# Optimization experiments

Hardware: AMD Instinct MI355X
Metric: run time of the kernel (lower is better)

The kernel has to match this reference:

```python
import jax, jax.numpy as jnp
import numpy as np

N, T, H = 307, 256, 64
NH, DH = 4, 16  # transformer heads, head dim (64/4)


def _layernorm(x, g, b, eps=1e-5):
    mu = x.mean(-1, keepdims=True)
    var = ((x - mu) ** 2).mean(-1, keepdims=True)
    return (x - mu) / jnp.sqrt(var + eps) * g + b


def _run_cell(x, m, tf, tj, Anorm, W0, b0, W1, mixW, mixb, Wih, Whh, bih, bhh, outW, outb, jamW, jamb):
    # x,m,tf,tj: [N,T]. Per-timestep 4-path ChebConv(K=2) + softmax mixing + GRUCell.
    hidden = Whh.shape[1]

    def step(h, xs):
        x_t, m_t, tf_t, tj_t = xs  # each [N]
        msg_in = jnp.concatenate([h, m_t[:, None], tf_t[:, None], tj_t[:, None]], axis=-1)  # [N,H+3]
        am = Anorm @ msg_in  # [N,H+3]
        m_all = jnp.tanh(jnp.einsum('ni,poi->npo', msg_in, W0) + b0
                         + jnp.einsum('ni,poi->npo', am, W1))  # [N,4,H]
        mix = jax.nn.softmax(h @ mixW.T + mixb, axis=1)  # [N,4]
        msg = jnp.einsum('np,npo->no', mix, m_all)  # [N,H]
        inp = jnp.concatenate([msg, (x_t * m_t)[:, None], m_t[:, None]], axis=-1)  # [N,H+2]
        # PyTorch GRUCell (gate order r,z,n)
        gi = inp @ Wih.T + bih
        gh = h @ Whh.T + bhh
        i_r, i_z, i_n = jnp.split(gi, 3, axis=-1)
        h_r, h_z, h_n = jnp.split(gh, 3, axis=-1)
        r = jax.nn.sigmoid(i_r + h_r)
        z = jax.nn.sigmoid(i_z + h_z)
        n = jnp.tanh(i_n + r * h_n)
        h_new = (1.0 - z) * n + z * h
        h2 = h_new + 0.1 * h
        pred = (h2 @ outW.T + outb)[:, 0]
        jam = (h2 @ jamW.T + jamb)[:, 0]
        return h2, (pred, jam, h2)

    h0 = jnp.zeros((x.shape[0], hidden), x.dtype)
    _, (preds, jams, hs) = jax.lax.scan(step, h0, (x.T, m.T, tf.T, tj.T))
    return preds.T, jams.T, jnp.transpose(hs, (1, 0, 2))  # [N,T],[N,T],[N,T,H]


def _pos_enc(Tlen, hdim, dtype):
    pos = jnp.arange(Tlen, dtype=dtype)[:, None]
    div = 10000.0 ** (jnp.arange(0, hdim, 2, dtype=dtype) / hdim)
    pe = jnp.zeros((Tlen, hdim), dtype)
    pe = pe.at[:, 0::2].set(jnp.sin(pos / div))
    pe = pe.at[:, 1::2].set(jnp.cos(pos / div))
    return pe


def _enhancer(h, qkvW, qkvb, oW, ob, g1, be1, f1W, f1b, f2W, f2b, g2, be2, pW, pb):
    # h: [N,T,H]; post-norm TransformerEncoder (relu, no dropout at eval), then Linear(H,1)
    x = h + _pos_enc(h.shape[1], h.shape[2], h.dtype)[None]
    n_layers = qkvW.shape[0]
    for l in range(n_layers):
        qkv = x @ qkvW[l].T + qkvb[l]
        q, k, v = jnp.split(qkv, 3, axis=-1)
        sh = (x.shape[0], x.shape[1], NH, DH)
        q, k, v = q.reshape(sh), k.reshape(sh), v.reshape(sh)
        att = jax.nn.softmax(jnp.einsum('nqhd,nkhd->nhqk', q, k) / np.sqrt(DH).astype(np.float32), axis=-1)
        o = jnp.einsum('nhqk,nkhd->nqhd', att, v).reshape(x.shape)
        o = o @ oW[l].T + ob[l]
        x = _layernorm(x + o, g1[l], be1[l])
        f = jax.nn.relu(x @ f1W[l].T + f1b[l]) @ f2W[l].T + f2b[l]
        x = _layernorm(x + f, g2[l], be2[l])
    return (x @ pW.T + pb)[..., 0]  # [N,T]


def _forward(x_seq, m_seq, tod_free, tod_jam, Anorm,
             cell_chebW0, cell_chebb0, cell_chebW1, cell_mixW, cell_mixb,
             cell_Wih, cell_Whh, cell_bih, cell_bhh,
             cell_outW, cell_outb, cell_jamW, cell_jamb,
             fuse_W1, fuse_b1, fuse_W2, fuse_b2,
             tr_qkvW, tr_qkvb, tr_oW, tr_ob, tr_ln1g, tr_ln1b,
             tr_ff1W, tr_ff1b, tr_ff2W, tr_ff2b, tr_ln2g, tr_ln2b,
             tr_projW, tr_projb):
    def cell(i, x, m, tf, tj):
        return _run_cell(x, m, tf, tj, Anorm,
                         cell_chebW0[i], cell_chebb0[i], cell_chebW1[i],
                         cell_mixW[i], cell_mixb[i],
                         cell_Wih[i], cell_Whh[i], cell_bih[i], cell_bhh[i],
                         cell_outW[i], cell_outb[i], cell_jamW[i], cell_jamb[i])

    flip = lambda a: a[:, ::-1]
    pf, jf, h_fwd = cell(0, x_seq, m_seq, tod_free, tod_jam)
    pb_r, jb_r, h_bwd_r = cell(1, flip(x_seq), flip(m_seq), flip(tod_free), flip(tod_jam))
    pb, jb, h_bwd = flip(pb_r), flip(jb_r), h_bwd_r[:, ::-1]

    fuse_in = jnp.stack([pf, pb], axis=-1)  # [N,T,2]
    w = jax.nn.softmax(jax.nn.relu(fuse_in @ fuse_W1.T + fuse_b1) @ fuse_W2.T + fuse_b2, axis=-1)
    speed = w[..., 0] * pf + w[..., 1] * pb
    jam_logit = w[..., 0] * jf + w[..., 1] * jb

    h_fused = h_fwd * w[..., 0:1] + h_bwd * w[..., 1:2]  # [N,T,H]
    args = lambda i: (tr_qkvW[i], tr_qkvb[i], tr_oW[i], tr_ob[i], tr_ln1g[i], tr_ln1b[i],
                      tr_ff1W[i], tr_ff1b[i], tr_ff2W[i], tr_ff2b[i], tr_ln2g[i], tr_ln2b[i],
                      tr_projW[i], tr_projb[i])
    speed_refined = _enhancer(h_fused, *args(0))
    jam_refined = _enhancer(h_fused, *args(1))
    alpha = 0.3
    speed = (1.0 - alpha) * speed + alpha * speed_refined
    jam_logit = (1.0 - alpha) * jam_logit + alpha * jam_refined
    return speed, jam_logit


def setup_inputs() -> dict:
    key = jax.random.key(0)
    keys = list(jax.random.split(key, 40))
    kit = iter(keys)

    def rn(shape, s=0.05):
        return s * jax.random.normal(next(kit), shape, jnp.float32)

    # sparse gaussian-normalized adjacency -> row-normalized diffusion matrix
    rng = np.random.default_rng(0)
    d = rng.uniform(0.5, 3.0, (N, N)); d = (d + d.T) / 2
    keep = rng.uniform(size=(N, N)) < 0.05; keep = keep | keep.T
    d = np.where(keep, d, np.inf)
    sigma = d[d < np.inf].std() + 1e-8
    adj = np.where(d < np.inf, np.exp(-d ** 2 / sigma ** 2), 0.0)
    np.fill_diagonal(adj, 1.0)
    dinv = np.where(adj.sum(1) > 0, (adj.sum(1) + 1e-8) ** -0.5, 0.0)
    adj_sym = adj * dinv[:, None] * dinv[None, :]
    rowsum = adj_sym.sum(1)
    Anorm = (adj_sym * np.where(rowsum > 0, 1.0 / rowsum, 0.0)[:, None]).astype(np.float32)

    inp = {
        'x_seq': jax.random.normal(next(kit), (N, T), jnp.float32),
        'm_seq': (jax.random.uniform(next(kit), (N, T)) < 0.5).astype(jnp.float32),
        'tod_free': jax.random.uniform(next(kit), (N, T), jnp.float32),
        'tod_jam': jax.random.uniform(next(kit), (N, T), jnp.float32),
        'Anorm': jnp.asarray(Anorm),
        'cell_chebW0': rn((2, 4, H, H + 3)), 'cell_chebb0': jnp.zeros((2, 4, H), jnp.float32),
        'cell_chebW1': rn((2, 4, H, H + 3)),
        'cell_mixW': rn((2, 4, H)), 'cell_mixb': jnp.zeros((2, 4), jnp.float32),
        'cell_Wih': rn((2, 3 * H, H + 2)), 'cell_Whh': rn((2, 3 * H, H)),
        'cell_bih': jnp.zeros((2, 3 * H), jnp.float32), 'cell_bhh': jnp.zeros((2, 3 * H), jnp.float32),
        'cell_outW': rn((2, 1, H)), 'cell_outb': jnp.zeros((2, 1), jnp.float32),
        'cell_jamW': rn((2, 1, H)), 'cell_jamb': jnp.zeros((2, 1), jnp.float32),
        'fuse_W1': rn((H, 2)), 'fuse_b1': jnp.zeros((H,), jnp.float32),
        'fuse_W2': rn((2, H)), 'fuse_b2': jnp.zeros((2,), jnp.float32),
        'tr_qkvW': rn((2, 3, 3 * H, H)), 'tr_qkvb': jnp.zeros((2, 3, 3 * H), jnp.float32),
        'tr_oW': rn((2, 3, H, H)), 'tr_ob': jnp.zeros((2, 3, H), jnp.float32),
        'tr_ln1g': jnp.ones((2, 3, H), jnp.float32), 'tr_ln1b': jnp.zeros((2, 3, H), jnp.float32),
        'tr_ff1W': rn((2, 3, 256, H)), 'tr_ff1b': jnp.zeros((2, 3, 256), jnp.float32),
        'tr_ff2W': rn((2, 3, H, 256)), 'tr_ff2b': jnp.zeros((2, 3, H), jnp.float32),
        'tr_ln2g': jnp.ones((2, 3, H), jnp.float32), 'tr_ln2b': jnp.zeros((2, 3, H), jnp.float32),
        'tr_projW': rn((2, 1, H)), 'tr_projb': jnp.zeros((2, 1), jnp.float32),
    }
    return inp


def reference(x_seq, m_seq, tod_free, tod_jam, Anorm,
              cell_chebW0, cell_chebb0, cell_chebW1, cell_mixW, cell_mixb,
              cell_Wih, cell_Whh, cell_bih, cell_bhh,
              cell_outW, cell_outb, cell_jamW, cell_jamb,
              fuse_W1, fuse_b1, fuse_W2, fuse_b2,
              tr_qkvW, tr_qkvb, tr_oW, tr_ob, tr_ln1g, tr_ln1b,
              tr_ff1W, tr_ff1b, tr_ff2W, tr_ff2b, tr_ln2g, tr_ln2b,
              tr_projW, tr_projb):
    return _forward(x_seq, m_seq, tod_free, tod_jam, Anorm,
                    cell_chebW0, cell_chebb0, cell_chebW1, cell_mixW, cell_mixb,
                    cell_Wih, cell_Whh, cell_bih, cell_bhh,
                    cell_outW, cell_outb, cell_jamW, cell_jamb,
                    fuse_W1, fuse_b1, fuse_W2, fuse_b2,
                    tr_qkvW, tr_qkvb, tr_oW, tr_ob, tr_ln1g, tr_ln1b,
                    tr_ff1W, tr_ff1b, tr_ff2W, tr_ff2b, tr_ln2g, tr_ln2b,
                    tr_projW, tr_projb)
```

## Files before the change

### kernel.cpp

```cpp
#include <hip/hip_runtime.h>
#include <math.h>

#define NN   307
#define TT   256
#define HHH  64
#define NROW (NN*TT)
#define NBLK_D 77
#define SCANB  154

typedef unsigned short u16;
typedef __attribute__((ext_vector_type(8))) short short8;
typedef __attribute__((ext_vector_type(4))) float f4;

__device__ __forceinline__ float wsum(float v){
#pragma unroll
  for (int off = 32; off > 0; off >>= 1) v += __shfl_xor(v, off, 64);
  return v;
}
__device__ __forceinline__ float wsum16(float v){
#pragma unroll
  for (int off = 8; off > 0; off >>= 1) v += __shfl_xor(v, off, 64);
  return v;
}
__device__ __forceinline__ float ftanh(float x){
  x = fminf(20.f, fmaxf(-20.f, x));
  float e = __expf(2.f*x);
  return (e - 1.f)/(e + 1.f);
}
__device__ __forceinline__ float fsigm(float x){ return 1.f/(1.f + __expf(-x)); }

__device__ __forceinline__ u16 f2bf(float x){
  unsigned u = __float_as_uint(x);
  u += 0x7fffu + ((u >> 16) & 1u);
  return (u16)(u >> 16);
}
__device__ __forceinline__ void split8(const float* xv, short8& hi, short8& lo){
  union { short8 v; u16 u[8]; } H, L;
#pragma unroll
  for (int j = 0; j < 8; j++){
    const float x = xv[j];
    const u16 h = f2bf(x);
    H.u[j] = h;
    L.u[j] = f2bf(x - __uint_as_float((unsigned)h << 16));
  }
  hi = H.v; lo = L.v;
}

__global__ void k_sparse(const float* __restrict__ A, int* __restrict__ cnt,
                         int* __restrict__ idx, float* __restrict__ val){
  int n = blockIdx.x*64 + threadIdx.x;
  if (n >= NN) return;
  int c = 0;
  for (int m = 0; m < NN; m++){
    float a = A[n*NN + m];
    if (a != 0.f){ idx[n*NN + c] = m; val[n*NN + c] = a; c++; }
  }
  cnt[n] = c;
}

__global__ void k_tr_cheb(const float* __restrict__ W0, const float* __restrict__ W1,
                          float* __restrict__ W0T, float* __restrict__ W1T){
  int t = blockIdx.x*256 + threadIdx.x;
  if (t >= 2*67*256) return;
  int c = t & 255; int rest = t >> 8; int i = rest % 67; int d = rest / 67;
  int p = c >> 6, o = c & 63;
  int src = ((d*4 + p)*64 + o)*67 + i;
  W0T[t] = W0[src];
  W1T[t] = W1[src];
}

__global__ void k_tr_gru(const float* __restrict__ Wih, const float* __restrict__ Whh,
                         float* __restrict__ WihT, float* __restrict__ WhhT){
  int t = blockIdx.x*256 + threadIdx.x;
  if (t < 2*66*192){
    int j = t % 192; int rest = t / 192; int i = rest % 66; int d = rest / 66;
    WihT[t] = Wih[(d*192 + j)*66 + i];
  }
  if (t < 2*64*192){
    int j = t % 192; int rest = t / 192; int i = rest % 64; int d = rest / 64;
    WhhT[t] = Whh[(d*192 + j)*64 + i];
  }
}

__global__ void k_af(const float* __restrict__ mseq, const float* __restrict__ tfr,
                     const float* __restrict__ tjm, const int* __restrict__ cnt,
                     const int* __restrict__ idx, const float* __restrict__ val,
                     float* __restrict__ AF){
  int n = blockIdx.x, c = blockIdx.y, t = threadIdx.x;
  const float* feat = (c == 0) ? mseq : (c == 1) ? tfr : tjm;
  float acc = 0.f; int k = cnt[n];
  for (int s = 0; s < k; s++) acc += val[n*NN + s] * feat[idx[n*NN + s]*TT + t];
  AF[((size_t)c*NN + n)*TT + t] = acc;
}

__global__ void k_split(const float* __restrict__ src, u16* __restrict__ hi,
                        u16* __restrict__ lo, int n){
  int i = blockIdx.x*256 + threadIdx.x;
  if (i >= n) return;
  const float x = src[i];
  const u16 h = f2bf(x);
  hi[i] = h;
  lo[i] = f2bf(x - __uint_as_float((unsigned)h << 16));
}

__global__ __launch_bounds__(256, 1)
void k_scan(const float* __restrict__ xseq, const float* __restrict__ mseq,
            const float* __restrict__ tfr, const float* __restrict__ tjm,
            const float* __restrict__ W0T, const float* __restrict__ W1T,
            const float* __restrict__ b0g,
            const float* __restrict__ mixW, const float* __restrict__ mixb,
            const float* __restrict__ WihT, const float* __restrict__ WhhT,
            const float* __restrict__ bih, const float* __restrict__ bhh,
            const float* __restrict__ outW, const float* __restrict__ outb,
            const float* __restrict__ jamW, const float* __restrict__ jamb,
            const int* __restrict__ spcnt, const int* __restrict__ spidx,
            const float* __restrict__ spval, const float* __restrict__ AF,
            float* __restrict__ Hseq, float* __restrict__ PRED, float* __restrict__ JPRED,
            int* __restrict__ slots)
{
  const int tid = threadIdx.x;
  const int bid = blockIdx.x;
  const int d   = bid / NBLK_D;
  const int n0  = (bid % NBLK_D) * 4;
  const int lane = tid & 63;
  const int wid  = tid >> 6;

  __shared__ __align__(16) float hsT[64][4];
  __shared__ __align__(16) float amsT[68][4];
  __shared__ __align__(16) float msgsT[64][4];
  __shared__ float malls[256][5];
  __shared__ float gis[4][192];
  __shared__ float ghs[4][192];
  __shared__ float mixs[4][4];
  __shared__ float xss[4], mss[4], tfs[4], tjs[4];
  __shared__ int   s_idx[4][320];
  __shared__ float s_val[4][320];
  __shared__ int   s_cnt[4];

  float w0r[67], w1r[67];
#pragma unroll
  for (int i = 0; i < 67; i++){
    w0r[i] = W0T[(d*67 + i)*256 + tid];
    w1r[i] = W1T[(d*67 + i)*256 + tid];
  }
  const float b0r = b0g[d*256 + tid];
  float wih_r[64], whh_r[64];
  float wih64 = 0.f, wih65 = 0.f, bih_r = 0.f, bhh_r = 0.f;
  if (tid < 192){
#pragma unroll
    for (int i = 0; i < 64; i++){
      whh_r[i] = WhhT[(d*64 + i)*192 + tid];
      wih_r[i] = WihT[(d*66 + i)*192 + tid];
    }
    wih64 = WihT[(d*66 + 64)*192 + tid];
    wih65 = WihT[(d*66 + 65)*192 + tid];
    bih_r = bih[d*192 + tid];
    bhh_r = bhh[d*192 + tid];
  }
  float mixw_r[4];
#pragma unroll
  for (int p = 0; p < 4; p++) mixw_r[p] = mixW[(d*4 + p)*64 + lane];
  const float mixb0 = mixb[d*4+0], mixb1 = mixb[d*4+1], mixb2 = mixb[d*4+2], mixb3 = mixb[d*4+3];
  const float outw_r = outW[d*64 + lane], jamw_r = jamW[d*64 + lane];
  const float outb_r = outb[d], jamb_r = jamb[d];

  for (int r = 0; r < 4; r++){
    const int n = min(n0 + r, NN-1);
    const int cc = spcnt[n];
    const int ccp = (cc + 15) & ~15;
    if (tid == 0) s_cnt[r] = ccp;
    for (int s = tid; s < ccp; s += 256){
      s_idx[r][s] = (s < cc) ? spidx[n*NN + s] : 0;
      s_val[r][s] = (s < cc) ? spval[n*NN + s] : 0.f;
    }
  }
  hsT[lane][wid] = 0.f;
  __syncthreads();

#pragma unroll 1
  for (int k = 0; k < TT; k++){
    const int ts = (d == 0) ? k : (TT-1 - k);
    if (tid < 4){
      const int r = tid; const int n = min(n0 + r, NN-1);
      const float mv = mseq[n*TT + ts];
      mss[r] = mv; tfs[r] = tfr[n*TT + ts]; tjs[r] = tjm[n*TT + ts];
      xss[r] = xseq[n*TT + ts];
      amsT[64][r] = AF[(0*NN + n)*TT + ts];
      amsT[65][r] = AF[(1*NN + n)*TT + ts];
      amsT[66][r] = AF[(2*NN + n)*TT + ts];
    }
    {
      const int r = wid;
      const float hv = hsT[lane][r];
      float l0 = wsum(hv * mixw_r[0]) + mixb0;
      float l1 = wsum(hv * mixw_r[1]) + mixb1;
      float l2 = wsum(hv * mixw_r[2]) + mixb2;
      float l3 = wsum(hv * mixw_r[3]) + mixb3;
      const float mx = fmaxf(fmaxf(l0,l1), fmaxf(l2,l3));
      const float e0 = __expf(l0-mx), e1 = __expf(l1-mx), e2 = __expf(l2-mx), e3 = __expf(l3-mx);
      const float inv = 1.f/(e0+e1+e2+e3);
      if (lane == 0){
        mixs[0][r] = e0*inv; mixs[1][r] = e1*inv; mixs[2][r] = e2*inv; mixs[3][r] = e3*inv;
      }
    }
    __syncthreads();
    {
      float a0 = b0r, a1 = b0r, a2 = b0r, a3 = b0r;
#pragma unroll
      for (int i = 0; i < 64; i++){
        const float4 h4 = *(const float4*)&hsT[i][0];
        const float w = w0r[i];
        a0 += h4.x*w; a1 += h4.y*w; a2 += h4.z*w; a3 += h4.w*w;
      }
      a0 += mss[0]*w0r[64] + tfs[0]*w0r[65] + tjs[0]*w0r[66];
      a1 += mss[1]*w0r[64] + tfs[1]*w0r[65] + tjs[1]*w0r[66];
      a2 += mss[2]*w0r[64] + tfs[2]*w0r[65] + tjs[2]*w0r[66];
      a3 += mss[3]*w0r[64] + tfs[3]*w0r[65] + tjs[3]*w0r[66];
      malls[tid][0] = a0; malls[tid][1] = a1; malls[tid][2] = a2; malls[tid][3] = a3;
    }
    if (tid < 192){
      float g0 = bhh_r, g1 = bhh_r, g2 = bhh_r, g3 = bhh_r;
#pragma unroll
      for (int i = 0; i < 64; i++){
        const float4 h4 = *(const float4*)&hsT[i][0];
        const float w = whh_r[i];
        g0 += h4.x*w; g1 += h4.y*w; g2 += h4.z*w; g3 += h4.w*w;
      }
      ghs[0][tid] = g0; ghs[1][tid] = g1; ghs[2][tid] = g2; ghs[3][tid] = g3;
      gis[0][tid] = bih_r + (xss[0]*mss[0])*wih64 + mss[0]*wih65;
      gis[1][tid] = bih_r + (xss[1]*mss[1])*wih64 + mss[1]*wih65;
      gis[2][tid] = bih_r + (xss[2]*mss[2])*wih64 + mss[2]*wih65;
      gis[3][tid] = bih_r + (xss[3]*mss[3])*wih64 + mss[3]*wih65;
    }
    if (k > 0 && tid < 64){
      const int* sl = slots + (size_t)d*NBLK_D*16;
      const int i2 = lane + 64;
      for (;;){
        const int va = (lane < NBLK_D)
            ? __hip_atomic_load(&sl[lane*16], __ATOMIC_RELAXED, __HIP_MEMORY_SCOPE_AGENT)
            : 0x7fffffff;
        const int vb = (i2 < NBLK_D)
            ? __hip_atomic_load(&sl[i2*16], __ATOMIC_RELAXED, __HIP_MEMORY_SCOPE_AGENT)
            : 0x7fffffff;
        if (__all(min(va, vb) >= k)) break;
        __builtin_amdgcn_s_sleep(1);
      }
    }
    __syncthreads();
    {
      const float* Hprev = Hseq + (size_t)(d*257 + k)*NN*64;
      const int r = wid;
      const int ccp = s_cnt[r];
      float acc = 0.f;
      for (int s = 0; s < ccp; s += 16){
        float aV[16], hV[16];
#pragma unroll
        for (int u = 0; u < 16; u++){
          const int m = s_idx[r][s+u];
          aV[u] = s_val[r][s+u];
          hV[u] = __hip_atomic_load(&Hprev[(size_t)m*64 + lane],
                                    __ATOMIC_RELAXED, __HIP_MEMORY_SCOPE_AGENT);
        }
#pragma unroll
        for (int u = 0; u < 16; u++) acc += aV[u]*hV[u];
      }
      amsT[lane][r] = acc;
    }
    __syncthreads();
    {
      const int p = tid >> 6;
      float pa0 = malls[tid][0], pa1 = malls[tid][1], pa2 = malls[tid][2], pa3 = malls[tid][3];
#pragma unroll
      for (int i = 0; i < 67; i++){
        const float4 m4 = *(const float4*)&amsT[i][0];
        const float w = w1r[i];
        pa0 += m4.x*w; pa1 += m4.y*w; pa2 += m4.z*w; pa3 += m4.w*w;
      }
      malls[tid][0] = mixs[p][0]*ftanh(pa0);
      malls[tid][1] = mixs[p][1]*ftanh(pa1);
      malls[tid][2] = mixs[p][2]*ftanh(pa2);
      malls[tid][3] = mixs[p][3]*ftanh(pa3);
    }
    __syncthreads();
    msgsT[lane][wid] = malls[lane][wid] + malls[64+lane][wid] + malls[128+lane][wid] + malls[192+lane][wid];
    __syncthreads();
    if (tid < 192){
      float q0 = gis[0][tid], q1 = gis[1][tid], q2 = gis[2][tid], q3 = gis[3][tid];
#pragma unroll
      for (int i = 0; i < 64; i++){
        const float4 m4 = *(const float4*)&msgsT[i][0];
        const float w = wih_r[i];
        q0 += m4.x*w; q1 += m4.y*w; q2 += m4.z*w; q3 += m4.w*w;
      }
      gis[0][tid] = q0; gis[1][tid] = q1; gis[2][tid] = q2; gis[3][tid] = q3;
    }
    __syncthreads();
    {
      const int r = wid, o = lane;
      const float ir = gis[r][o], iz = gis[r][o+64], in_ = gis[r][o+128];
      const float hr = ghs[r][o], hz = ghs[r][o+64], hn = ghs[r][o+128];
      const float rr2 = fsigm(ir + hr);
      const float zz = fsigm(iz + hz);
      const float nnv = ftanh(in_ + rr2*hn);
      const float hold = hsT[o][r];
      const float h2 = (1.f - zz)*nnv + zz*hold + 0.1f*hold;
      hsT[o][r] = h2;
      const int n = n0 + r;
      if (n < NN)
        __hip_atomic_store(&Hseq[((size_t)(d*257 + k + 1)*NN + n)*64 + o], h2,
                           __ATOMIC_RELAXED, __HIP_MEMORY_SCOPE_AGENT);
    }
    __syncthreads();
    if (tid == 0)
      __hip_atomic_store(&slots[bid*16], k + 1, __ATOMIC_RELAXED, __HIP_MEMORY_SCOPE_AGENT);
    {
      const float h2 = hsT[lane][wid];
      const float pv = wsum(h2 * outw_r);
      const float jv = wsum(h2 * jamw_r);
      const int n = n0 + wid;
      if (lane == 0 && n < NN){
        PRED [(d*NN + n)*TT + ts] = pv + outb_r;
        JPRED[(d*NN + n)*TT + ts] = jv + jamb_r;
      }
    }
  }
}

__global__ __launch_bounds__(256)
void k_fusion(const float* __restrict__ PRED, const float* __restrict__ JPRED,
              const float* __restrict__ Hseq,
              const float* __restrict__ fw1, const float* __restrict__ fb1,
              const float* __restrict__ fw2, const float* __restrict__ fb2,
              float* __restrict__ x0, float* __restrict__ outp)
{
  const int tid = threadIdx.x;
  const int rr = tid >> 6, lane = tid & 63;
  const int idx = blockIdx.x*4 + rr;
  const int n = idx >> 8, t = idx & 255;
  const float pf = PRED[(0*NN + n)*TT + t], pb = PRED[(NN + n)*TT + t];
  const float jf = JPRED[(0*NN + n)*TT + t], jb = JPRED[(NN + n)*TT + t];
  const float hid = fmaxf(fw1[lane*2]*pf + fw1[lane*2+1]*pb + fb1[lane], 0.f);
  const float l0 = wsum(hid * fw2[lane]) + fb2[0];
  const float l1 = wsum(hid * fw2[64+lane]) + fb2[1];
  const float mx = fmaxf(l0,l1);
  const float e0 = __expf(l0-mx), e1 = __expf(l1-mx);
  const float inv = 1.f/(e0+e1);
  const float w0 = e0*inv, w1 = e1*inv;
  const float hf = Hseq[((size_t)(0*257 + t + 1)*NN + n)*64 + lane];
  const float hb = Hseq[((size_t)(257 + 256 - t)*NN + n)*64 + lane];
  const int i2 = lane & ~1;
  const float dv = powf(10000.f, (float)i2 * (1.f/64.f));
  const float arg = (float)t / dv;
  const float pe = (lane & 1) ? cosf(arg) : sinf(arg);
  x0[(size_t)idx*64 + lane] = hf*w0 + hb*w1 + pe;
  if (lane == 0){
    outp[idx]        = 0.7f*(w0*pf + w1*pb);
    outp[NROW + idx] = 0.7f*(w0*jf + w1*jb);
  }
}

__global__ __launch_bounds__(256)
void k_qkv(const float* __restrict__ X, const u16* __restrict__ Whi,
           const u16* __restrict__ Wlo, const float* __restrict__ bias,
           float* __restrict__ Y)
{
  const int tid = threadIdx.x;
  const int w = tid >> 6, l = tid & 63;
  const int m16 = l & 15, q = l >> 4;
  const int row = blockIdx.x*64 + w*16 + m16;
  short8 Ah[2], Al[2];
#pragma unroll
  for (int kh = 0; kh < 2; kh++){
    float xv[8];
    *(float4*)&xv[0] = *(const float4*)&X[(size_t)row*64 + kh*32 + q*8];
    *(float4*)&xv[4] = *(const float4*)&X[(size_t)row*64 + kh*32 + q*8 + 4];
    split8(xv, Ah[kh], Al[kh]);
  }
  const int rbase = blockIdx.x*64 + w*16 + q*4;
  for (int nt = 0; nt < 12; nt++){
    const int n = nt*16 + m16;
    f4 acc = {0.f, 0.f, 0.f, 0.f};
#pragma unroll
    for (int kh = 0; kh < 2; kh++){
      const short8 Bh = *(const short8*)&Whi[(size_t)n*64 + kh*32 + q*8];
      const short8 Bl = *(const short8*)&Wlo[(size_t)n*64 + kh*32 + q*8];
      acc = __builtin_amdgcn_mfma_f32_16x16x32_bf16(Ah[kh], Bh, acc, 0, 0, 0);
      acc = __builtin_amdgcn_mfma_f32_16x16x32_bf16(Ah[kh], Bl, acc, 0, 0, 0);
      acc = __builtin_amdgcn_mfma_f32_16x16x32_bf16(Al[kh], Bh, acc, 0, 0, 0);
    }
    const float bb = bias[n];
#pragma unroll
    for (int r = 0; r < 4; r++)
      Y[(size_t)(rbase + r)*192 + n] = acc[r] + bb;
  }
}

__global__ __launch_bounds__(256)
void k_oproj_ln(const float* __restrict__ X, const u16* __restrict__ Whi,
                const u16* __restrict__ Wlo, const float* __restrict__ bias,
                const float* __restrict__ Xres, const float* __restrict__ g,
                const float* __restrict__ b, float* __restrict__ Y)
{
  const int tid = threadIdx.x;
  const int w = tid >> 6, l = tid & 63;
  const int m16 = l & 15, q = l >> 4;
  const int row = blockIdx.x*64 + w*16 + m16;
  short8 Ah[2], Al[2];
#pragma unroll
  for (int kh = 0; kh < 2; kh++){
    float xv[8];
    *(float4*)&xv[0] = *(const float4*)&X[(size_t)row*64 + kh*32 + q*8];
    *(float4*)&xv[4] = *(const float4*)&X[(size_t)row*64 + kh*32 + q*8 + 4];
    split8(xv, Ah[kh], Al[kh]);
  }
  f4 acc[4];
#pragma unroll
  for (int nt = 0; nt < 4; nt++){
    acc[nt] = (f4){0.f, 0.f, 0.f, 0.f};
    const int n = nt*16 + m16;
#pragma unroll
    for (int kh = 0; kh < 2; kh++){
      const short8 Bh = *(const short8*)&Whi[(size_t)n*64 + kh*32 + q*8];
      const short8 Bl = *(const short8*)&Wlo[(size_t)n*64 + kh*32 + q*8];
      acc[nt] = __builtin_amdgcn_mfma_f32_16x16x32_bf16(Ah[kh], Bh, acc[nt], 0, 0, 0);
      acc[nt] = __builtin_amdgcn_mfma_f32_16x16x32_bf16(Ah[kh], Bl, acc[nt], 0, 0, 0);
      acc[nt] = __builtin_amdgcn_mfma_f32_16x16x32_bf16(Al[kh], Bh, acc[nt], 0, 0, 0);
    }
  }
  const int rbase = blockIdx.x*64 + w*16 + q*4;
#pragma unroll
  for (int r = 0; r < 4; r++){
    float v[4]; float s = 0.f;
#pragma unroll
    for (int nt = 0; nt < 4; nt++){
      const int col = nt*16 + m16;
      v[nt] = acc[nt][r] + bias[col] + Xres[(size_t)(rbase + r)*64 + col];
      s += v[nt];
    }
    const float mu = wsum16(s) * (1.f/64.f);
    float vs = 0.f;
#pragma unroll
    for (int nt = 0; nt < 4; nt++){ v[nt] -= mu; vs += v[nt]*v[nt]; }
    const float rstd = rsqrtf(wsum16(vs) * (1.f/64.f) + 1e-5f);
#pragma unroll
    for (int nt = 0; nt < 4; nt++){
      const int col = nt*16 + m16;
      Y[(size_t)(rbase + r)*64 + col] = v[nt] * rstd * g[col] + b[col];
    }
  }
}

__global__ __launch_bounds__(256)
void k_ffblock(const float* __restrict__ X,
               const u16* __restrict__ W1hi, const u16* __restrict__ W1lo,
               const float* __restrict__ b1,
               const u16* __restrict__ W2hi, const u16* __restrict__ W2lo,
               const float* __restrict__ b2,
               const float* __restrict__ g, const float* __restrict__ b,
               float* __restrict__ Y)
{
  __shared__ __align__(16) u16 Hs[64][280];
  const int tid = threadIdx.x;
  const int w = tid >> 6, l = tid & 63;
  const int m16 = l & 15, q = l >> 4;
  const int row = blockIdx.x*64 + w*16 + m16;
  short8 Ah[2], Al[2];
#pragma unroll
  for (int kh = 0; kh < 2; kh++){
    float xv[8];
    *(float4*)&xv[0] = *(const float4*)&X[(size_t)row*64 + kh*32 + q*8];
    *(float4*)&xv[4] = *(const float4*)&X[(size_t)row*64 + kh*32 + q*8 + 4];
    split8(xv, Ah[kh], Al[kh]);
  }
  for (int nt = 0; nt < 16; nt++){
    const int n = nt*16 + m16;
    f4 acc = {0.f, 0.f, 0.f, 0.f};
#pragma unroll
    for (int kh = 0; kh < 2; kh++){
      const short8 Bh = *(const short8*)&W1hi[(size_t)n*64 + kh*32 + q*8];
      const short8 Bl = *(const short8*)&W1lo[(size_t)n*64 + kh*32 + q*8];
      acc = __builtin_amdgcn_mfma_f32_16x16x32_bf16(Ah[kh], Bh, acc, 0, 0, 0);
      acc = __builtin_amdgcn_mfma_f32_16x16x32_bf16(Ah[kh], Bl, acc, 0, 0, 0);
      acc = __builtin_amdgcn_mfma_f32_16x16x32_bf16(Al[kh], Bh, acc, 0, 0, 0);
    }
    const float bb = b1[n];
#pragma unroll
    for (int r = 0; r < 4; r++){
      const float h = fmaxf(acc[r] + bb, 0.f);
      Hs[w*16 + q*4 + r][n] = f2bf(h);
    }
  }
  __syncthreads();
  f4 acc2[4];
#pragma unroll
  for (int nt = 0; nt < 4; nt++) acc2[nt] = (f4){0.f, 0.f, 0.f, 0.f};
#pragma unroll 1
  for (int kh = 0; kh < 8; kh++){
    const short8 Ahh = *(const short8*)&Hs[w*16 + m16][kh*32 + q*8];
#pragma unroll
    for (int nt = 0; nt < 4; nt++){
      const int n = nt*16 + m16;
      const short8 Bh = *(const short8*)&W2hi[(size_t)n*256 + kh*32 + q*8];
      const short8 Bl = *(const short8*)&W2lo[(size_t)n*256 + kh*32 + q*8];
      acc2[nt] = __builtin_amdgcn_mfma_f32_16x16x32_bf16(Ahh, Bh, acc2[nt], 0, 0, 0);
      acc2[nt] = __builtin_amdgcn_mfma_f32_16x16x32_bf16(Ahh, Bl, acc2[nt], 0, 0, 0);
    }
  }
  const int rbase = blockIdx.x*64 + w*16 + q*4;
#pragma unroll
  for (int r = 0; r < 4; r++){
    float v[4]; float s = 0.f;
#pragma unroll
    for (int nt = 0; nt < 4; nt++){
      const int col = nt*16 + m16;
      v[nt] = acc2[nt][r] + b2[col] + X[(size_t)(rbase + r)*64 + col];
      s += v[nt];
    }
    const float mu = wsum16(s) * (1.f/64.f);
    float vs = 0.f;
#pragma unroll
    for (int nt = 0; nt < 4; nt++){ v[nt] -= mu; vs += v[nt]*v[nt]; }
    const float rstd = rsqrtf(wsum16(vs) * (1.f/64.f) + 1e-5f);
#pragma unroll
    for (int nt = 0; nt < 4; nt++){
      const int col = nt*16 + m16;
      Y[(size_t)(rbase + r)*64 + col] = v[nt] * rstd * g[col] + b[col];
    }
  }
}

__global__ __launch_bounds__(256)
void k_attn(const float* __restrict__ QKV, float* __restrict__ O)
{
  const int n = blockIdx.x, h = blockIdx.y;
  const int tid = threadIdx.x;
  __shared__ __align__(16) float Ks[256][20];
  __shared__ __align__(16) float Vs[256][20];
  const float* nbase = QKV + (size_t)n*256*192;
  {
    const int part = tid & 7;
    const int kv = part >> 2;
    const int c4 = (part & 3) * 4;
#pragma unroll
    for (int p = 0; p < 8; p++){
      const int t = p*32 + (tid >> 3);
      const float4 v4 = *(const float4*)(nbase + (size_t)t*192 + 64 + kv*64 + h*16 + c4);
      if (kv == 0) *(float4*)&Ks[t][c4] = v4;
      else         *(float4*)&Vs[t][c4] = v4;
    }
  }
  float q[16];
  {
    const float4* qs = (const float4*)(nbase + (size_t)tid*192 + h*16);
#pragma unroll
    for (int c = 0; c < 4; c++){
      float4 t4 = qs[c];
      q[c*4+0]=t4.x*0.25f; q[c*4+1]=t4.y*0.25f; q[c*4+2]=t4.z*0.25f; q[c*4+3]=t4.w*0.25f;
    }
  }
  __syncthreads();
  float l = 0.f, acc[16] = {};
  for (int j = 0; j < 256; j++){
    float s = 0.f;
#pragma unroll
    for (int dd = 0; dd < 16; dd++) s += q[dd]*Ks[j][dd];
    const float p = __expf(s);
    l += p;
#pragma unroll
    for (int dd = 0; dd < 16; dd++) acc[dd] += p*Vs[j][dd];
  }
  const float inv = 1.f/l;
  float* orow = O + ((size_t)n*256 + tid)*64 + h*16;
#pragma unroll
  for (int dd = 0; dd < 16; dd++) orow[dd] = acc[dd]*inv;
}

__global__ __launch_bounds__(256)
void k_proj_add(const float* __restrict__ X, const float* __restrict__ pW,
                const float* __restrict__ pb, float* __restrict__ outp)
{
  const int tid = threadIdx.x;
  const int r = tid >> 6, lane = tid & 63;
  const size_t row = (size_t)blockIdx.x*4 + r;
  const float v = X[row*64 + lane] * pW[lane];
  const float s = wsum(v);
  if (lane == 0) outp[row] += 0.3f*(s + pb[0]);
}

extern "C" void kernel_launch(void* const* d_in, const int* in_sizes, int n_in,
                              void* d_out, int out_size, void* d_ws, size_t ws_size,
                              hipStream_t stream)
{
  const float* x_seq = (const float*)d_in[0];
  const float* m_seq = (const float*)d_in[1];
  const float* tod_f = (const float*)d_in[2];
  const float* tod_j = (const float*)d_in[3];
  const float* Anorm = (const float*)d_in[4];
  const float* chW0  = (const float*)d_in[5];
  const float* chb0  = (const float*)d_in[6];
  const float* chW1  = (const float*)d_in[7];
  const float* mixW  = (const float*)d_in[8];
  const float* mixb  = (const float*)d_in[9];
  const float* Wih   = (const float*)d_in[10];
  const float* Whh   = (const float*)d_in[11];
  const float* bih   = (const float*)d_in[12];
  const float* bhh   = (const float*)d_in[13];
  const float* outW  = (const float*)d_in[14];
  const float* outbp = (const float*)d_in[15];
  const float* jamW  = (const float*)d_in[16];
  const float* jambp = (const float*)d_in[17];
  const float* fW1   = (const float*)d_in[18];
  const float* fb1   = (const float*)d_in[19];
  const float* fW2   = (const float*)d_in[20];
  const float* fb2   = (const float*)d_in[21];
  const float* qkvW  = (const float*)d_in[22];
  const float* qkvb  = (const float*)d_in[23];
  const float* oW    = (const float*)d_in[24];
  const float* ob    = (const float*)d_in[25];
  const float* ln1g  = (const float*)d_in[26];
  const float* ln1b  = (const float*)d_in[27];
  const float* f1W   = (const float*)d_in[28];
  const float* f1b   = (const float*)d_in[29];
  const float* f2W   = (const float*)d_in[30];
  const float* f2b   = (const float*)d_in[31];
  const float* ln2g  = (const float*)d_in[32];
  const float* ln2b  = (const float*)d_in[33];
  const float* prW   = (const float*)d_in[34];
  const float* prb   = (const float*)d_in[35];
  float* out = (float*)d_out;

  float* ws = (float*)d_ws;
  size_t off = 0;
  auto take = [&](size_t n)->float*{ float* p = ws + off; off += (n + 63) & ~(size_t)63; return p; };
  int*   slots = (int*)take(4096);
  float* W0T  = take((size_t)2*67*256);
  float* W1T  = take((size_t)2*67*256);
  float* WihT = take((size_t)2*66*192);
  float* WhhT = take((size_t)2*64*192);
  int*   spcnt = (int*)take(320);
  int*   spidx = (int*)take((size_t)NN*NN);
  float* spval = take((size_t)NN*NN);
  float* AF    = take((size_t)3*NN*TT);
  float* PRED  = take((size_t)2*NN*TT);
  float* JPRED = take((size_t)2*NN*TT);
  float* HSEQ  = take((size_t)2*257*NN*64);
  float* X0    = take((size_t)NROW*64);
  float* XBUF  = take((size_t)NROW*64);
  float* OBUF  = take((size_t)NROW*64);
  float* FBUF  = take((size_t)NROW*256);
  const size_t NQKV = (size_t)6*192*64;
  const size_t NO   = (size_t)6*64*64;
  const size_t NF1  = (size_t)6*256*64;
  const size_t NF2  = (size_t)6*64*256;
  const size_t NWTOT = NQKV + NO + NF1 + NF2;
  u16* WHI = (u16*)take((NWTOT + 1)/2);
  u16* WLO = (u16*)take((NWTOT + 1)/2);
  (void)ws_size; (void)in_sizes; (void)n_in; (void)out_size;

  hipMemsetAsync(slots, 0, 4096*sizeof(int), stream);
  hipMemsetAsync(HSEQ, 0, (size_t)NN*64*sizeof(float), stream);
  hipMemsetAsync(HSEQ + (size_t)257*NN*64, 0, (size_t)NN*64*sizeof(float), stream);

  k_sparse<<<dim3((NN+63)/64), dim3(64), 0, stream>>>(Anorm, spcnt, spidx, spval);
  k_tr_cheb<<<dim3(134), dim3(256), 0, stream>>>(chW0, chW1, W0T, W1T);
  k_tr_gru<<<dim3(99), dim3(256), 0, stream>>>(Wih, Whh, WihT, WhhT);
  k_af<<<dim3(NN,3), dim3(256), 0, stream>>>(m_seq, tod_f, tod_j, spcnt, spidx, spval, AF);
  k_split<<<dim3((int)((NQKV+255)/256)), dim3(256), 0, stream>>>(qkvW, WHI, WLO, (int)NQKV);
  k_split<<<dim3((int)((NO+255)/256)), dim3(256), 0, stream>>>(oW, WHI+NQKV, WLO+NQKV, (int)NO);
  k_split<<<dim3((int)((NF1+255)/256)), dim3(256), 0, stream>>>(f1W, WHI+NQKV+NO, WLO+NQKV+NO, (int)NF1);
  k_split<<<dim3((int)((NF2+255)/256)), dim3(256), 0, stream>>>(f2W, WHI+NQKV+NO+NF1, WLO+NQKV+NO+NF1, (int)NF2);

  k_scan<<<dim3(SCANB), dim3(256), 0, stream>>>(x_seq, m_seq, tod_f, tod_j, W0T, W1T,
      chb0, mixW, mixb, WihT, WhhT, bih, bhh, outW, outbp, jamW, jambp,
      spcnt, spidx, spval, AF, HSEQ, PRED, JPRED, slots);

  k_fusion<<<dim3(NROW/4), dim3(256), 0, stream>>>(PRED, JPRED, HSEQ, fW1, fb1, fW2, fb2, X0, out);

  for (int e = 0; e < 2; e++){
    for (int l = 0; l < 3; l++){
      const int el = e*3 + l;
      const float* xin = (l == 0) ? X0 : XBUF;
      const u16* qhi = WHI + (size_t)el*192*64;
      const u16* qlo = WLO + (size_t)el*192*64;
      const u16* ohi = WHI + NQKV + (size_t)el*64*64;
      const u16* olo = WLO + NQKV + (size_t)el*64*64;
      const u16* f1hi = WHI + NQKV + NO + (size_t)el*256*64;
      const u16* f1lo = WLO + NQKV + NO + (size_t)el*256*64;
      const u16* f2hi = WHI + NQKV + NO + NF1 + (size_t)el*64*256;
      const u16* f2lo = WLO + NQKV + NO + NF1 + (size_t)el*64*256;
      k_qkv<<<dim3(NROW/64), dim3(256), 0, stream>>>(xin, qhi, qlo,
          qkvb + (size_t)el*192, FBUF);
      k_attn<<<dim3(NN, 4), dim3(256), 0, stream>>>(FBUF, OBUF);
      k_oproj_ln<<<dim3(NROW/64), dim3(256), 0, stream>>>(OBUF, ohi, olo,
          ob + (size_t)el*64, xin, ln1g + (size_t)el*64, ln1b + (size_t)el*64, XBUF);
      k_ffblock<<<dim3(NROW/64), dim3(256), 0, stream>>>(XBUF, f1hi, f1lo,
          f1b + (size_t)el*256, f2hi, f2lo, f2b + (size_t)el*64,
          ln2g + (size_t)el*64, ln2b + (size_t)el*64, XBUF);
    }
    k_proj_add<<<dim3(NROW/4), dim3(256), 0, stream>>>(XBUF, prW + (size_t)e*64, prb + e,
        out + (size_t)e*NROW);
  }
}
```

Measured before the change: 4.959 ms.

## Rewrite attention kernel to use bf16 MFMA with split-precision QK and shared P/V

```diff
diff --git a/kernel.cpp b/kernel.cpp
--- a/kernel.cpp
+++ b/kernel.cpp
@@ -532,47 +532,75 @@
 __global__ __launch_bounds__(256)
 void k_attn(const float* __restrict__ QKV, float* __restrict__ O)
 {
-  const int n = blockIdx.x, h = blockIdx.y;
+  __shared__ __align__(16) u16 Vst[4][16][264];
+  __shared__ __align__(16) u16 Pst[4][16][264];
+  const int n = blockIdx.x;
   const int tid = threadIdx.x;
-  __shared__ __align__(16) float Ks[256][20];
-  __shared__ __align__(16) float Vs[256][20];
+  const int h = tid >> 6;
+  const int l = tid & 63;
+  const int m16 = l & 15, q = l >> 4;
   const float* nbase = QKV + (size_t)n*256*192;
-  {
-    const int part = tid & 7;
-    const int kv = part >> 2;
-    const int c4 = (part & 3) * 4;
-#pragma unroll
-    for (int p = 0; p < 8; p++){
-      const int t = p*32 + (tid >> 3);
-      const float4 v4 = *(const float4*)(nbase + (size_t)t*192 + 64 + kv*64 + h*16 + c4);
-      if (kv == 0) *(float4*)&Ks[t][c4] = v4;
-      else         *(float4*)&Vs[t][c4] = v4;
-    }
-  }
-  float q[16];
-  {
-    const float4* qs = (const float4*)(nbase + (size_t)tid*192 + h*16);
-#pragma unroll
-    for (int c = 0; c < 4; c++){
-      float4 t4 = qs[c];
-      q[c*4+0]=t4.x*0.25f; q[c*4+1]=t4.y*0.25f; q[c*4+2]=t4.z*0.25f; q[c*4+3]=t4.w*0.25f;
-    }
+  const short8 z8 = {0,0,0,0,0,0,0,0};
+
+  for (int kb = 0; kb < 64; kb++){
+    const int key = kb*4 + q;
+    const float vv = nbase[(size_t)key*192 + 128 + h*16 + m16];
+    Vst[h][m16][key] = f2bf(vv);
+  }
+  short8 Bh[16], Bl[16];
+#pragma unroll
+  for (int ct = 0; ct < 16; ct++){
+    if (q < 2){
+      float kv[8];
+      *(float4*)&kv[0] = *(const float4*)&nbase[(size_t)(ct*16+m16)*192 + 64 + h*16 + q*8];
+      *(float4*)&kv[4] = *(const float4*)&nbase[(size_t)(ct*16+m16)*192 + 64 + h*16 + q*8 + 4];
+      split8(kv, Bh[ct], Bl[ct]);
+    } else { Bh[ct] = z8; Bl[ct] = z8; }
   }
   __syncthreads();
-  float l = 0.f, acc[16] = {};
-  for (int j = 0; j < 256; j++){
-    float s = 0.f;
-#pragma unroll
-    for (int dd = 0; dd < 16; dd++) s += q[dd]*Ks[j][dd];
-    const float p = __expf(s);
-    l += p;
-#pragma unroll
-    for (int dd = 0; dd < 16; dd++) acc[dd] += p*Vs[j][dd];
-  }
-  const float inv = 1.f/l;
-  float* orow = O + ((size_t)n*256 + tid)*64 + h*16;
-#pragma unroll
-  for (int dd = 0; dd < 16; dd++) orow[dd] = acc[dd]*inv;
+
+#pragma unroll 1
+  for (int c = 0; c < 16; c++){
+    const int c0 = c*16;
+    short8 Qh, Ql;
+    if (q < 2){
+      float xv[8];
+      *(float4*)&xv[0] = *(const float4*)&nbase[(size_t)(c0+m16)*192 + h*16 + q*8];
+      *(float4*)&xv[4] = *(const float4*)&nbase[(size_t)(c0+m16)*192 + h*16 + q*8 + 4];
+#pragma unroll
+      for (int j2 = 0; j2 < 8; j2++) xv[j2] *= 0.25f;
+      split8(xv, Qh, Ql);
+    } else { Qh = z8; Ql = z8; }
+    float rs[4] = {0.f, 0.f, 0.f, 0.f};
+#pragma unroll
+    for (int ct = 0; ct < 16; ct++){
+      f4 s = {0.f, 0.f, 0.f, 0.f};
+      s = __builtin_amdgcn_mfma_f32_16x16x32_bf16(Qh, Bh[ct], s, 0, 0, 0);
+      s = __builtin_amdgcn_mfma_f32_16x16x32_bf16(Qh, Bl[ct], s, 0, 0, 0);
+      s = __builtin_amdgcn_mfma_f32_16x16x32_bf16(Ql, Bh[ct], s, 0, 0, 0);
+#pragma unroll
+      for (int r = 0; r < 4; r++){
+        const float p = __expf(s[r]);
+        rs[r] += p;
+        Pst[h][q*4 + r][ct*16 + m16] = f2bf(p);
+      }
+    }
+#pragma unroll
+    for (int r = 0; r < 4; r++) rs[r] = wsum16(rs[r]);
+    __syncthreads();
+    f4 acc = {0.f, 0.f, 0.f, 0.f};
+#pragma unroll
+    for (int kt = 0; kt < 8; kt++){
+      const short8 Pa = *(const short8*)&Pst[h][m16][kt*32 + q*8];
+      const short8 Vb = *(const short8*)&Vst[h][m16][kt*32 + q*8];
+      acc = __builtin_amdgcn_mfma_f32_16x16x32_bf16(Pa, Vb, acc, 0, 0, 0);
+    }
+    __syncthreads();
+#pragma unroll
+    for (int r = 0; r < 4; r++){
+      O[((size_t)n*256 + c0 + q*4 + r)*64 + h*16 + m16] = acc[r] / rs[r];
+    }
+  }
 }
 
 __global__ __launch_bounds__(256)
@@ -690,7 +718,7 @@
       const u16* f2lo = WLO + NQKV + NO + NF1 + (size_t)el*64*256;
       k_qkv<<<dim3(NROW/64), dim3(256), 0, stream>>>(xin, qhi, qlo,
           qkvb + (size_t)el*192, FBUF);
-      k_attn<<<dim3(NN, 4), dim3(256), 0, stream>>>(FBUF, OBUF);
+      k_attn<<<dim3(NN), dim3(256), 0, stream>>>(FBUF, OBUF);
       k_oproj_ln<<<dim3(NROW/64), dim3(256), 0, stream>>>(OBUF, ohi, olo,
           ob + (size_t)el*64, xin, ln1g + (size_t)el*64, ln1b + (size_t)el*64, XBUF);
       k_ffblock<<<dim3(NROW/64), dim3(256), 0, stream>>>(XBUF, f1hi, f1lo,
```

Result: faster. 4.773 ms (-3.8%).
